# Kernel tuning notes

Measured on AMD Instinct MI355X. Metric: run time of the kernel, lower is better.

## Reference

```python
import jax, jax.numpy as jnp
import numpy as np

HN, ND, STRIDE, ESTRIDE = 10, 40, 3, 3  # hidden_node, ndim, stride, encode_stride


def _build_graphs():
    # Dense aggregation matrices A[dst, src] equivalent to the module's fixed
    # edge lists (scatter-add of src features into dst). Graph is tiny (10/40
    # nodes) and identical across the batch, so dense matmul is the efficient
    # exact form of the gather->scatter-add.
    w = np.float32(np.exp(-(1.0 / STRIDE) ** 2))
    A_pred = np.zeros((HN, HN), np.float32)
    for j in range(HN):
        A_pred[j, j] += 1.0                      # edge [j, j], weight 1
        for dj in range(1, STRIDE - 1):          # dj = 1 only
            A_pred[(j - dj) % HN, j] += w        # edge [j, j-dj]
            A_pred[(j + dj) % HN, j] += w        # edge [j, j+dj]
    A_enc = np.zeros((HN, ND), np.float32)
    A_dec = np.zeros((ND, HN), np.float32)
    for j in range(HN):
        cg = (j * ND // HN) % ND                 # center_grid = 4j
        for i in range(cg - ESTRIDE, cg + ESTRIDE):
            A_enc[j, i % ND] += 1.0              # grid i -> hidden j
            A_dec[i % ND, j] += 1.0              # hidden j -> grid i
    return jnp.asarray(A_enc), jnp.asarray(A_pred), jnp.asarray(A_dec)

A_ENC, A_PRED, A_DEC = _build_graphs()


def setup_inputs() -> dict:
    key = jax.random.key(0)
    ks = jax.random.split(key, 12)
    B, HF = 524288, 8
    s = 0.3  # modest weight scale
    return {
        "x": jax.random.normal(ks[0], (B, ND), jnp.float32),
        "z": jax.random.uniform(ks[1], (B, HN, HF), dtype=jnp.float32),
        "y": jax.random.uniform(ks[2], (B, ND, 1), dtype=jnp.float32),
        "enc_rel_w": jax.random.normal(ks[3], (HF, 1), jnp.float32) * s,
        "enc_rel_b": jax.random.normal(ks[4], (HF,), jnp.float32) * s,
        "enc_root_w": jax.random.normal(ks[5], (HF, HF), jnp.float32) * s,
        "pred_rel_w": jax.random.normal(ks[6], (HF, HF), jnp.float32) * s,
        "pred_rel_b": jax.random.normal(ks[7], (HF,), jnp.float32) * s,
        "pred_root_w": jax.random.normal(ks[8], (HF, HF), jnp.float32) * s,
        "dec_rel_w": jax.random.normal(ks[9], (1, HF), jnp.float32) * s,
        "dec_rel_b": jax.random.normal(ks[10], (1,), jnp.float32) * s,
        "dec_root_w": jax.random.normal(ks[11], (1, 1), jnp.float32) * s,
    }


def reference(x, z, y, enc_rel_w, enc_rel_b, enc_root_w,
              pred_rel_w, pred_rel_b, pred_root_w,
              dec_rel_w, dec_rel_b, dec_root_w):
    xb = x[..., None]  # [B, 40, 1]
    # encoder GraphConv((1, 8) -> 8): lin_rel(agg(x_src)) + lin_root(z)
    agg = jnp.einsum('ds,bsf->bdf', A_ENC, xb)                 # [B, 10, 1]
    z1 = jax.nn.relu(agg @ enc_rel_w.T + enc_rel_b + z @ enc_root_w.T)
    # predictor GraphConv(8 -> 8) with edge weights folded into A_PRED
    agg2 = jnp.einsum('ds,bsf->bdf', A_PRED, z1)               # [B, 10, 8]
    z2 = jax.nn.relu(agg2 @ pred_rel_w.T + pred_rel_b + z1 @ pred_root_w.T)
    # decoder GraphConv((8, 1) -> 1)
    agg3 = jnp.einsum('ds,bsf->bdf', A_DEC, z2)                # [B, 40, 8]
    out = agg3 @ dec_rel_w.T + dec_rel_b + y @ dec_root_w.T   # [B, 40, 1]
    return out[..., 0]                                         # [B, 40]
```

## Files before the change

kernel.cpp:

```cpp
#include <hip/hip_runtime.h>


#define HN 10
#define ND 40
#define HF 8
#define TPB 64
#define ROW4 11

__global__ __launch_bounds__(TPB) void gnn_kernel(
    const float* __restrict__ x,
    const float* __restrict__ z,
    const float* __restrict__ y,
    const float* __restrict__ enc_rel_w,
    const float* __restrict__ enc_rel_b,
    const float* __restrict__ enc_root_w,
    const float* __restrict__ pred_rel_w,
    const float* __restrict__ pred_rel_b,
    const float* __restrict__ pred_root_w,
    const float* __restrict__ dec_rel_w,
    const float* __restrict__ dec_rel_b,
    const float* __restrict__ dec_root_w,
    float* __restrict__ out,
    int B)
{
    __shared__ float4 lds4[TPB * ROW4];
    const int t = threadIdx.x;
    const long long tile = (long long)blockIdx.x * TPB;

    const float w = 0.8948393168143698f;

    const float4* xg = (const float4*)(x + tile * ND);
    #pragma unroll
    for (int k = 0; k < 10; ++k) {
        int i = t + TPB * k;
        int e = i / 10, q = i - e * 10;
        lds4[e * ROW4 + q] = xg[i];
    }
    __syncthreads();

    float agg[HN];
    {
        float xv[ND];
        #pragma unroll
        for (int k = 0; k < 10; ++k) {
            float4 v = lds4[t * ROW4 + k];
            xv[4*k+0] = v.x; xv[4*k+1] = v.y; xv[4*k+2] = v.z; xv[4*k+3] = v.w;
        }
        agg[0] = xv[37] + xv[38] + xv[39] + xv[0] + xv[1] + xv[2];
        #pragma unroll
        for (int j = 1; j < HN; ++j)
            agg[j] = xv[4*j-3] + xv[4*j-2] + xv[4*j-1] + xv[4*j] + xv[4*j+1] + xv[4*j+2];
    }
    __syncthreads();

    auto enc_row = [&](int jj, int j, float (&r)[HF]) {
        float4 v0 = lds4[t * ROW4 + jj * 2];
        float4 v1 = lds4[t * ROW4 + jj * 2 + 1];
        float zr[HF] = {v0.x, v0.y, v0.z, v0.w, v1.x, v1.y, v1.z, v1.w};
        #pragma unroll
        for (int f = 0; f < HF; ++f) {
            float acc = agg[j] * enc_rel_w[f] + enc_rel_b[f];
            #pragma unroll
            for (int g = 0; g < HF; ++g)
                acc += zr[g] * enc_root_w[f * HF + g];
            r[f] = fmaxf(acc, 0.0f);
        }
    };

    auto emit = [&](const float (&rm)[HF], const float (&rc)[HF],
                    const float (&rp)[HF]) -> float {
        float a2[HF];
        #pragma unroll
        for (int f = 0; f < HF; ++f)
            a2[f] = rc[f] + w * (rm[f] + rp[f]);
        float s = 0.0f;
        #pragma unroll
        for (int f = 0; f < HF; ++f) {
            float acc = pred_rel_b[f];
            #pragma unroll
            for (int g = 0; g < HF; ++g)
                acc += a2[g] * pred_rel_w[f * HF + g];
            #pragma unroll
            for (int g = 0; g < HF; ++g)
                acc += rc[g] * pred_root_w[f * HF + g];
            s += fmaxf(acc, 0.0f) * dec_rel_w[f];
        }
        return s;
    };

    const float4* zg = (const float4*)(z + tile * (HN * HF));
    float s2[HN];

    #pragma unroll
    for (int k = 0; k < 10; ++k) {
        int i = t + TPB * k;
        int e = i / 10, q = i - e * 10;
        lds4[e * ROW4 + q] = zg[e * 20 + q];
    }
    __syncthreads();

    float rA[5][HF];
    #pragma unroll
    for (int jj = 0; jj < 5; ++jj) enc_row(jj, jj, rA[jj]);
    s2[1] = emit(rA[0], rA[1], rA[2]);
    s2[2] = emit(rA[1], rA[2], rA[3]);
    s2[3] = emit(rA[2], rA[3], rA[4]);
    __syncthreads();

    #pragma unroll
    for (int k = 0; k < 10; ++k) {
        int i = t + TPB * k;
        int e = i / 10, q = i - e * 10;
        lds4[e * ROW4 + q] = zg[e * 20 + 10 + q];
    }
    __syncthreads();

    float rB[5][HF];
    #pragma unroll
    for (int jj = 0; jj < 5; ++jj) enc_row(jj, 5 + jj, rB[jj]);
    s2[4] = emit(rA[3], rA[4], rB[0]);
    s2[5] = emit(rA[4], rB[0], rB[1]);
    s2[6] = emit(rB[0], rB[1], rB[2]);
    s2[7] = emit(rB[1], rB[2], rB[3]);
    s2[8] = emit(rB[2], rB[3], rB[4]);
    s2[9] = emit(rB[3], rB[4], rA[0]);
    s2[0] = emit(rB[4], rA[0], rA[1]);
    __syncthreads();

    const float drb = dec_rel_b[0];
    const float droot = dec_root_w[0];
    #pragma unroll
    for (int k = 0; k < 10; ++k) {
        const int k1 = (k + 1) % HN;
        const float pair = s2[k] + s2[k1] + drb;
        float4 vo;
        vo.x = s2[k] + drb;
        vo.y = pair;
        vo.z = pair;
        vo.w = s2[k1] + drb;
        lds4[t * ROW4 + k] = vo;
    }
    __syncthreads();

    const float4* yg = (const float4*)(y + tile * ND);
    float4* og = (float4*)(out + tile * ND);
    #pragma unroll
    for (int k = 0; k < 10; ++k) {
        int i = t + TPB * k;
        int e = i / 10, q = i - e * 10;
        float4 p = lds4[e * ROW4 + q];
        float4 vy = yg[i];
        p.x += vy.x * droot;
        p.y += vy.y * droot;
        p.z += vy.z * droot;
        p.w += vy.w * droot;
        og[i] = p;
    }
}

extern "C" void kernel_launch(void* const* d_in, const int* in_sizes, int n_in,
                              void* d_out, int out_size, void* d_ws, size_t ws_size,
                              hipStream_t stream) {
    const float* x          = (const float*)d_in[0];
    const float* z          = (const float*)d_in[1];
    const float* y          = (const float*)d_in[2];
    const float* enc_rel_w  = (const float*)d_in[3];
    const float* enc_rel_b  = (const float*)d_in[4];
    const float* enc_root_w = (const float*)d_in[5];
    const float* pred_rel_w = (const float*)d_in[6];
    const float* pred_rel_b = (const float*)d_in[7];
    const float* pred_root_w= (const float*)d_in[8];
    const float* dec_rel_w  = (const float*)d_in[9];
    const float* dec_rel_b  = (const float*)d_in[10];
    const float* dec_root_w = (const float*)d_in[11];
    float* out = (float*)d_out;

    const int B = in_sizes[0] / ND;
    const int blocks = B / TPB;
    gnn_kernel<<<blocks, TPB, 0, stream>>>(
        x, z, y, enc_rel_w, enc_rel_b, enc_root_w,
        pred_rel_w, pred_rel_b, pred_root_w,
        dec_rel_w, dec_rel_b, dec_root_w, out, B);
}
```

Baseline: 423.5 us.

## Use per-wave LDS regions with waitcnt instead of block barriers; load z directly

```diff
diff --git a/kernel.cpp b/kernel.cpp
--- a/kernel.cpp
+++ b/kernel.cpp
@@ -4,7 +4,8 @@
 #define HN 10
 #define ND 40
 #define HF 8
-#define TPB 64
+#define TPB 256
+#define WLEN 64
 #define ROW4 11
 
 __global__ __launch_bounds__(TPB) void gnn_kernel(
@@ -24,26 +25,30 @@
     int B)
 {
     __shared__ float4 lds4[TPB * ROW4];
-    const int t = threadIdx.x;
-    const long long tile = (long long)blockIdx.x * TPB;
+    const int t    = threadIdx.x;
+    const int lane = t & 63;
+    const int wv   = t >> 6;
+    const long long wbase = (long long)blockIdx.x * TPB + wv * WLEN;
+    float4* wl = lds4 + wv * (WLEN * ROW4);
 
     const float w = 0.8948393168143698f;
 
-    const float4* xg = (const float4*)(x + tile * ND);
+    const float4* xg = (const float4*)(x + wbase * ND);
     #pragma unroll
     for (int k = 0; k < 10; ++k) {
-        int i = t + TPB * k;
+        int i = lane + WLEN * k;
         int e = i / 10, q = i - e * 10;
-        lds4[e * ROW4 + q] = xg[i];
+        wl[e * ROW4 + q] = xg[i];
     }
-    __syncthreads();
+    asm volatile("s_waitcnt lgkmcnt(0)" ::: "memory");
+    __builtin_amdgcn_sched_barrier(0);
 
     float agg[HN];
     {
         float xv[ND];
         #pragma unroll
         for (int k = 0; k < 10; ++k) {
-            float4 v = lds4[t * ROW4 + k];
+            float4 v = wl[lane * ROW4 + k];
             xv[4*k+0] = v.x; xv[4*k+1] = v.y; xv[4*k+2] = v.z; xv[4*k+3] = v.w;
         }
         agg[0] = xv[37] + xv[38] + xv[39] + xv[0] + xv[1] + xv[2];
@@ -51,11 +56,15 @@
         for (int j = 1; j < HN; ++j)
             agg[j] = xv[4*j-3] + xv[4*j-2] + xv[4*j-1] + xv[4*j] + xv[4*j+1] + xv[4*j+2];
     }
-    __syncthreads();
 
-    auto enc_row = [&](int jj, int j, float (&r)[HF]) {
-        float4 v0 = lds4[t * ROW4 + jj * 2];
-        float4 v1 = lds4[t * ROW4 + jj * 2 + 1];
+    const float4* zrow = (const float4*)(z + (wbase + lane) * (HN * HF));
+    float4 zA[10], zB[10];
+    #pragma unroll
+    for (int k = 0; k < 10; ++k) zA[k] = zrow[k];
+    #pragma unroll
+    for (int k = 0; k < 10; ++k) zB[k] = zrow[10 + k];
+
+    auto enc_row = [&](float4 v0, float4 v1, int j, float (&r)[HF]) {
         float zr[HF] = {v0.x, v0.y, v0.z, v0.w, v1.x, v1.y, v1.z, v1.w};
         #pragma unroll
         for (int f = 0; f < HF; ++f) {
@@ -88,36 +97,16 @@
         return s;
     };
 
-    const float4* zg = (const float4*)(z + tile * (HN * HF));
+    float rA[5][HF], rB[5][HF];
+    #pragma unroll
+    for (int jj = 0; jj < 5; ++jj) enc_row(zA[2*jj], zA[2*jj+1], jj, rA[jj]);
+    #pragma unroll
+    for (int jj = 0; jj < 5; ++jj) enc_row(zB[2*jj], zB[2*jj+1], 5 + jj, rB[jj]);
+
     float s2[HN];
-
-    #pragma unroll
-    for (int k = 0; k < 10; ++k) {
-        int i = t + TPB * k;
-        int e = i / 10, q = i - e * 10;
-        lds4[e * ROW4 + q] = zg[e * 20 + q];
-    }
-    __syncthreads();
-
-    float rA[5][HF];
-    #pragma unroll
-    for (int jj = 0; jj < 5; ++jj) enc_row(jj, jj, rA[jj]);
     s2[1] = emit(rA[0], rA[1], rA[2]);
     s2[2] = emit(rA[1], rA[2], rA[3]);
     s2[3] = emit(rA[2], rA[3], rA[4]);
-    __syncthreads();
-
-    #pragma unroll
-    for (int k = 0; k < 10; ++k) {
-        int i = t + TPB * k;
-        int e = i / 10, q = i - e * 10;
-        lds4[e * ROW4 + q] = zg[e * 20 + 10 + q];
-    }
-    __syncthreads();
-
-    float rB[5][HF];
-    #pragma unroll
-    for (int jj = 0; jj < 5; ++jj) enc_row(jj, 5 + jj, rB[jj]);
     s2[4] = emit(rA[3], rA[4], rB[0]);
     s2[5] = emit(rA[4], rB[0], rB[1]);
     s2[6] = emit(rB[0], rB[1], rB[2]);
@@ -125,9 +114,8 @@
     s2[8] = emit(rB[2], rB[3], rB[4]);
     s2[9] = emit(rB[3], rB[4], rA[0]);
     s2[0] = emit(rB[4], rA[0], rA[1]);
-    __syncthreads();
 
-    const float drb = dec_rel_b[0];
+    const float drb   = dec_rel_b[0];
     const float droot = dec_root_w[0];
     #pragma unroll
     for (int k = 0; k < 10; ++k) {
@@ -138,17 +126,18 @@
         vo.y = pair;
         vo.z = pair;
         vo.w = s2[k1] + drb;
-        lds4[t * ROW4 + k] = vo;
+        wl[lane * ROW4 + k] = vo;
     }
-    __syncthreads();
+    asm volatile("s_waitcnt lgkmcnt(0)" ::: "memory");
+    __builtin_amdgcn_sched_barrier(0);
 
-    const float4* yg = (const float4*)(y + tile * ND);
-    float4* og = (float4*)(out + tile * ND);
+    const float4* yg = (const float4*)(y + wbase * ND);
+    float4* og = (float4*)(out + wbase * ND);
     #pragma unroll
     for (int k = 0; k < 10; ++k) {
-        int i = t + TPB * k;
+        int i = lane + WLEN * k;
         int e = i / 10, q = i - e * 10;
-        float4 p = lds4[e * ROW4 + q];
+        float4 p = wl[e * ROW4 + q];
         float4 vy = yg[i];
         p.x += vy.x * droot;
         p.y += vy.y * droot;
```

Result: faster. 412.6 us (-2.6%).
